# Performance work log

Measured on AMD Instinct MI355X. Metric: run time of the kernel, lower is better.

Reference implementation:

```python
import jax, jax.numpy as jnp
import numpy as np

HIDDEN = 256
INPUT = 1
OUTPUT = 1
BATCH = 64
SEQ = 2048


def setup_inputs() -> dict:
    key = jax.random.key(0)
    ks = jax.random.split(key, 8)
    s_ih = 1.0 / np.sqrt(HIDDEN)  # torch nn.LSTM init: U(-1/sqrt(H), 1/sqrt(H))
    x = jax.random.normal(ks[0], (BATCH, SEQ, INPUT), dtype=jnp.float32)
    W_ih = jax.random.uniform(ks[1], (4 * HIDDEN, INPUT), jnp.float32, -s_ih, s_ih)
    W_hh = jax.random.uniform(ks[2], (4 * HIDDEN, HIDDEN), jnp.float32, -s_ih, s_ih)
    b_ih = jax.random.uniform(ks[3], (4 * HIDDEN,), jnp.float32, -s_ih, s_ih)
    b_hh = jax.random.uniform(ks[4], (4 * HIDDEN,), jnp.float32, -s_ih, s_ih)
    W_fc = jax.random.uniform(ks[5], (OUTPUT, HIDDEN), jnp.float32, -s_ih, s_ih)
    b_fc = jax.random.uniform(ks[6], (OUTPUT,), jnp.float32, -s_ih, s_ih)
    return {"x": x, "W_ih": W_ih, "W_hh": W_hh, "b_ih": b_ih,
            "b_hh": b_hh, "W_fc": W_fc, "b_fc": b_fc}


def reference(x, W_ih, W_hh, b_ih, b_hh, W_fc, b_fc):
    B, T, _ = x.shape
    H = W_hh.shape[1]
    # precompute input contribution to all gates: [B,T,4H] (input_dim=1)
    gx = jnp.einsum('bti,gi->btg', x, W_ih) + b_ih + b_hh
    gx_t = jnp.transpose(gx, (1, 0, 2))  # [T,B,4H] for scan over time
    h0 = jnp.zeros((B, H), x.dtype)
    c0 = jnp.zeros((B, H), x.dtype)

    def step(carry, g_t):
        h, c = carry
        gates = g_t + h @ W_hh.T                 # [B,4H]
        i, f, g, o = jnp.split(gates, 4, axis=-1)  # torch gate order i,f,g,o
        i = jax.nn.sigmoid(i)
        f = jax.nn.sigmoid(f)
        g = jnp.tanh(g)
        o = jax.nn.sigmoid(o)
        c = f * c + i * g
        h = o * jnp.tanh(c)
        return (h, c), h

    (h_n, c_n), hs = jax.lax.scan(step, (h0, c0), gx_t)
    out = jnp.transpose(hs, (1, 0, 2))           # [B,T,H]
    y = out @ W_fc.T + b_fc                      # fused linear head [B,T,1]
    return (y, (h_n[None], c_n[None]))           # match torch (num_layers=1, B, H)
```

## Files before the change

kernel.cpp:

```cpp
#include <hip/hip_runtime.h>
#include <hip/hip_fp16.h>

#define SEQT 2048
#define HID  256
#define NB   64

typedef int int32x4 __attribute__((ext_vector_type(4)));
typedef _Float16 h2 __attribute__((ext_vector_type(2)));

#define LOG2E 1.4426950408889634f
static __device__ __forceinline__ float sigf(float x) {
  return __builtin_amdgcn_rcpf(1.f + __builtin_amdgcn_exp2f(-LOG2E * x));
}
static __device__ __forceinline__ float tanhf_fast(float x) {
  float e = __builtin_amdgcn_exp2f(-2.f * LOG2E * fabsf(x));
  float r = (1.f - e) * __builtin_amdgcn_rcpf(1.f + e);
  return copysignf(r, x);
}
static __device__ __forceinline__ float max4(float4 f) {
  return fmaxf(fmaxf(fabsf(f.x), fabsf(f.y)), fmaxf(fabsf(f.z), fabsf(f.w)));
}

__global__ __attribute__((amdgpu_flat_work_group_size(1024, 1024),
                          amdgpu_waves_per_eu(4, 4)))
void lstm_main(const float* __restrict__ x, const float* __restrict__ Wih,
               const float* __restrict__ Whh, const float* __restrict__ bih,
               const float* __restrict__ bhh, float* __restrict__ out,
               unsigned* __restrict__ hist)
{
  __shared__ __align__(16) unsigned char qring[16 * 256];
  __shared__ __align__(16) unsigned      f16r[16 * 128];
  __shared__ float xs[SEQT];
  __shared__ float rowS[1024];

  const int t    = threadIdx.x;
  const int b    = blockIdx.x;
  const int v    = t >> 6;
  const int lane = t & 63;
  const int ko   = lane >> 4;
  const int lm   = lane & 15;
  const int ru   = lm & 3;
  const int u    = 16 * v + 4 * ko + ru;

  ((float2*)xs)[t] = ((const float2*)(x + (size_t)b * SEQT))[t];
  if (t < 64) ((unsigned*)qring)[15 * 64 + t] = 0u;

  int32x4 af[4][4];
#pragma unroll
  for (int q = 0; q < 4; ++q) {
    const int row = q * 256 + 16 * v + lm;
    const float* rp = Whh + (size_t)row * HID + 16 * ko;
    float mx = 1e-20f;
#pragma unroll
    for (int kt = 0; kt < 4; ++kt) {
      const float4* p = (const float4*)(rp + 64 * kt);
      mx = fmaxf(mx, fmaxf(fmaxf(max4(p[0]), max4(p[1])),
                           fmaxf(max4(p[2]), max4(p[3]))));
    }
    mx = fmaxf(mx, __shfl_xor(mx, 16, 64));
    mx = fmaxf(mx, __shfl_xor(mx, 32, 64));
    const float winv = 127.f / mx;
    if (ko == 0) rowS[row] = mx * (1.f / (127.f * 127.f));
#pragma unroll
    for (int kt = 0; kt < 4; ++kt) {
      const float4* p = (const float4*)(rp + 64 * kt);
      int32x4 vv;
#pragma unroll
      for (int d = 0; d < 4; ++d) {
        float4 f = p[d];
        int q0 = (int)__builtin_rintf(f.x * winv);
        int q1 = (int)__builtin_rintf(f.y * winv);
        int q2 = (int)__builtin_rintf(f.z * winv);
        int q3 = (int)__builtin_rintf(f.w * winv);
        vv[d] = (q0 & 255) | ((q1 & 255) << 8) | ((q2 & 255) << 16) | ((q3 & 255) << 24);
      }
      af[q][kt] = vv;
    }
  }

  float biasu[4], wihu[4];
#pragma unroll
  for (int q = 0; q < 4; ++q) {
    int row = q * 256 + u;
    biasu[q] = bih[row] + bhh[row];
    wihu[q]  = Wih[row];
  }
  __syncthreads();
  float Su[4];
#pragma unroll
  for (int q = 0; q < 4; ++q) Su[q] = rowS[q * 256 + u];

  unsigned* histb = hist + (size_t)b * SEQT * 128;
  float c = 0.f, h = 0.f;
  const int32x4 z4 = {0, 0, 0, 0};

  for (int s = 0; s < SEQT; ++s) {
    float xv = xs[s];
    const unsigned char* qs = qring + ((s + 15) & 15) * 256;
    int32x4 bf[4];
#pragma unroll
    for (int kt = 0; kt < 4; ++kt)
      bf[kt] = *(const int32x4*)(qs + 64 * kt + 16 * ko);

    int32x4 acc[4];
#pragma unroll
    for (int q = 0; q < 4; ++q)
      acc[q] = __builtin_amdgcn_mfma_i32_16x16x64_i8(af[q][0], bf[0], z4, 0, 0, 0);
#pragma unroll
    for (int kt = 1; kt < 4; ++kt)
#pragma unroll
      for (int q = 0; q < 4; ++q)
        acc[q] = __builtin_amdgcn_mfma_i32_16x16x64_i8(af[q][kt], bf[kt], acc[q], 0, 0, 0);

    float aq[4];
#pragma unroll
    for (int q = 0; q < 4; ++q) {
      int32x4 vv = acc[q];
      int e01 = (ru & 1) ? vv[1] : vv[0];
      int e23 = (ru & 1) ? vv[3] : vv[2];
      int gv  = (ru & 2) ? e23 : e01;
      aq[q] = __builtin_fmaf((float)gv, Su[q],
                             __builtin_fmaf(wihu[q], xv, biasu[q]));
    }

    float I = sigf(aq[0]), F = sigf(aq[1]), G = tanhf_fast(aq[2]), O = sigf(aq[3]);
    c = F * c + I * G;
    h = O * tanhf_fast(c);

    if (lm < 4) {
      int qv = (int)__builtin_rintf(h * 127.f);
      ((char*)qring)[(s & 15) * 256 + u]    = (char)qv;
      ((_Float16*)f16r)[(s & 15) * 256 + u] = (_Float16)h;
    }
    __syncthreads();

    if ((s & 15) == 15) {
      if (t < 512) {
        uint4 vv = *(const uint4*)(f16r + 4 * t);
        *(uint4*)(histb + (size_t)(s - 15) * 128 + 4 * t) = vv;
      }
      __syncthreads();
    }
  }

  if (lm < 4) {
    out[NB * SEQT + b * HID + u]            = h;
    out[NB * SEQT + NB * HID + b * HID + u] = c;
  }
}

__global__ __launch_bounds__(256) void lstm_head(
    const unsigned* __restrict__ hist, const float* __restrict__ Wfc,
    const float* __restrict__ bfc, float* __restrict__ y)
{
  int gw   = (blockIdx.x * 256 + threadIdx.x) >> 6;
  int lane = threadIdx.x & 63;
  uint2 hv = ((const uint2*)(hist + (size_t)gw * 128))[lane];
  float4 w = ((const float4*)Wfc)[lane];
  h2 p0 = __builtin_bit_cast(h2, hv.x);
  h2 p1 = __builtin_bit_cast(h2, hv.y);
  float s = (float)p0.x * w.x + (float)p0.y * w.y +
            (float)p1.x * w.z + (float)p1.y * w.w;
#pragma unroll
  for (int m = 32; m; m >>= 1) s += __shfl_xor(s, m, 64);
  if (lane == 0) y[gw] = s + bfc[0];
}

extern "C" void kernel_launch(void* const* d_in, const int* in_sizes, int n_in,
                              void* d_out, int out_size, void* d_ws, size_t ws_size,
                              hipStream_t stream)
{
  const float* x   = (const float*)d_in[0];
  const float* Wih = (const float*)d_in[1];
  const float* Whh = (const float*)d_in[2];
  const float* bih = (const float*)d_in[3];
  const float* bhh = (const float*)d_in[4];
  const float* Wfc = (const float*)d_in[5];
  const float* bfc = (const float*)d_in[6];
  float* out      = (float*)d_out;
  unsigned* hist  = (unsigned*)d_ws;

  (void)in_sizes; (void)n_in; (void)out_size; (void)ws_size;

  lstm_main<<<dim3(NB), dim3(1024), 0, stream>>>(x, Wih, Whh, bih, bhh, out, hist);
  lstm_head<<<dim3((NB * SEQT) / 4), dim3(256), 0, stream>>>(hist, Wfc, bfc, out);
}
```

Measured before the change: 1.780 ms.

## Spread LSTM gate activations across lane quads with DPP exchange

Each lane in a quad now computes a single gate's activation instead of one lane computing all four. The sigmoid is rewritten as a scaled tanh so every lane runs the same transcendental. The quad then combines i*g, f*c and o*tanh(c) through DPP quad permutes. This shrinks the serial per-step transcendental chain on the recurrent critical path, at the cost of extra cross-lane moves and selects.

New measurement: 1.679 ms. 5.7% less time.

```diff
diff --git a/kernel.cpp b/kernel.cpp
--- a/kernel.cpp
+++ b/kernel.cpp
@@ -9,9 +9,6 @@
 typedef _Float16 h2 __attribute__((ext_vector_type(2)));
 
 #define LOG2E 1.4426950408889634f
-static __device__ __forceinline__ float sigf(float x) {
-  return __builtin_amdgcn_rcpf(1.f + __builtin_amdgcn_exp2f(-LOG2E * x));
-}
 static __device__ __forceinline__ float tanhf_fast(float x) {
   float e = __builtin_amdgcn_exp2f(-2.f * LOG2E * fabsf(x));
   float r = (1.f - e) * __builtin_amdgcn_rcpf(1.f + e);
@@ -20,6 +17,13 @@
 static __device__ __forceinline__ float max4(float4 f) {
   return fmaxf(fmaxf(fabsf(f.x), fabsf(f.y)), fmaxf(fabsf(f.z), fabsf(f.w)));
 }
+template <int CTRL>
+static __device__ __forceinline__ float dppf(float v) {
+  int p = __builtin_amdgcn_update_dpp(0, __builtin_bit_cast(int, v), CTRL, 0xF, 0xF, true);
+  return __builtin_bit_cast(float, p);
+}
+#define QP_XOR1 0xB1
+#define QP_XOR2 0x4E
 
 __global__ __attribute__((amdgpu_flat_work_group_size(1024, 1024),
                           amdgpu_waves_per_eu(4, 4)))
@@ -39,8 +43,10 @@
   const int lane = t & 63;
   const int ko   = lane >> 4;
   const int lm   = lane & 15;
-  const int ru   = lm & 3;
+  const int ru   = lm >> 2;
+  const int g    = lm & 3;
   const int u    = 16 * v + 4 * ko + ru;
+  const int qm   = ((g & 1) << 1) | (g >> 1);
 
   ((float2*)xs)[t] = ((const float2*)(x + (size_t)b * SEQT))[t];
   if (t < 64) ((unsigned*)qring)[15 * 64 + t] = 0u;
@@ -78,17 +84,14 @@
     }
   }
 
-  float biasu[4], wihu[4];
-#pragma unroll
-  for (int q = 0; q < 4; ++q) {
-    int row = q * 256 + u;
-    biasu[q] = bih[row] + bhh[row];
-    wihu[q]  = Wih[row];
-  }
+  const int grow   = qm * 256 + u;
+  const float biasg = bih[grow] + bhh[grow];
+  const float wihg  = Wih[grow];
+  const float scg = (g == 1) ? 1.0f : 0.5f;
+  const float amg = (g == 1) ? 1.0f : 0.5f;
+  const float abg = (g == 1) ? 0.0f : 0.5f;
   __syncthreads();
-  float Su[4];
-#pragma unroll
-  for (int q = 0; q < 4; ++q) Su[q] = rowS[q * 256 + u];
+  const float Sg = rowS[grow];
 
   unsigned* histb = hist + (size_t)b * SEQT * 128;
   float c = 0.f, h = 0.f;
@@ -112,22 +115,28 @@
       for (int q = 0; q < 4; ++q)
         acc[q] = __builtin_amdgcn_mfma_i32_16x16x64_i8(af[q][kt], bf[kt], acc[q], 0, 0, 0);
 
-    float aq[4];
-#pragma unroll
-    for (int q = 0; q < 4; ++q) {
-      int32x4 vv = acc[q];
-      int e01 = (ru & 1) ? vv[1] : vv[0];
-      int e23 = (ru & 1) ? vv[3] : vv[2];
-      int gv  = (ru & 2) ? e23 : e01;
-      aq[q] = __builtin_fmaf((float)gv, Su[q],
-                             __builtin_fmaf(wihu[q], xv, biasu[q]));
-    }
+    int32x4 A01 = (g & 2) ? acc[1] : acc[0];
+    int32x4 A23 = (g & 2) ? acc[3] : acc[2];
+    int32x4 Ag  = (g & 1) ? A23 : A01;
+    int e01 = (ru & 1) ? Ag[1] : Ag[0];
+    int e23 = (ru & 1) ? Ag[3] : Ag[2];
+    int gv  = (ru & 2) ? e23 : e01;
 
-    float I = sigf(aq[0]), F = sigf(aq[1]), G = tanhf_fast(aq[2]), O = sigf(aq[3]);
-    c = F * c + I * G;
-    h = O * tanhf_fast(c);
+    float a   = __builtin_fmaf((float)gv, Sg, __builtin_fmaf(wihg, xv, biasg));
+    float act = __builtin_fmaf(tanhf_fast(a * scg), amg, abg);
 
-    if (lm < 4) {
+    float B1 = dppf<QP_XOR1>(act);
+    float Pp = act * B1;
+    float Pv = dppf<QP_XOR2>(Pp);
+    float Fv = (g & 1) ? B1 : act;
+    float cn = __builtin_fmaf(Fv, c, Pv);
+    float cb = dppf<QP_XOR2>(cn);
+    c = (g & 2) ? cn : cb;
+    float th = tanhf_fast(c);
+    float Ov = (g & 1) ? act : B1;
+    h = Ov * th;
+
+    if (g == 3) {
       int qv = (int)__builtin_rintf(h * 127.f);
       ((char*)qring)[(s & 15) * 256 + u]    = (char)qv;
       ((_Float16*)f16r)[(s & 15) * 256 + u] = (_Float16)h;
@@ -143,7 +152,7 @@
     }
   }
 
-  if (lm < 4) {
+  if (g == 3) {
     out[NB * SEQT + b * HID + u]            = h;
     out[NB * SEQT + NB * HID + b * HID + u] = c;
   }
```
